# Kernel optimization log

Hardware: AMD Instinct MI355X
Metric: run time of the kernel (lower is better)

Reference implementation:

```python
import jax, jax.numpy as jnp
import numpy as np

T, DIM, HID = 8192, 1024, 4096

def setup_inputs() -> dict:
    key = jax.random.key(0)
    k1, k2, k3 = jax.random.split(key, 3)
    x = jax.random.normal(k1, (T, DIM), dtype=jnp.float32)
    # torch Linear weight layout: [out_features, in_features]
    W_fc = jax.random.normal(k2, (HID, DIM), dtype=jnp.float32) * 0.02
    W_proj = jax.random.normal(k3, (DIM, HID), dtype=jnp.float32) * 0.02
    return {"x": x, "W_fc": W_fc, "W_proj": W_proj}

def reference(x, W_fc, W_proj):
    # fc: x @ W_fc^T  -> relu -> square -> proj: @ W_proj^T
    h = jnp.einsum('td,hd->th', x, W_fc)      # [T, HID]
    h = jnp.square(jax.nn.relu(h))            # relu(h)^2 (relu^2 activation)
    return jnp.einsum('th,dh->td', h, W_proj) # [T, DIM]
```

## Files before the change

kernel.cpp:

```cpp
#include <hip/hip_runtime.h>
#include <stdint.h>


typedef __attribute__((ext_vector_type(8))) short bf16x8;
typedef __attribute__((ext_vector_type(4))) float f32x4;

typedef const __attribute__((address_space(1))) unsigned int* gas_u32p;
typedef __attribute__((address_space(3))) unsigned int* las_u32p;

__device__ __forceinline__ void load16_to_lds(const void* gptr, void* lptr) {
    __builtin_amdgcn_global_load_lds((gas_u32p)gptr, (las_u32p)lptr, 16, 0, 0);
}

__device__ __forceinline__ void dsr128(bf16x8& d, unsigned off) {
    asm volatile("ds_read_b128 %0, %1" : "=v"(d) : "v"(off));
}

__device__ __forceinline__ unsigned short f2bf(float f) {
    unsigned int u = __float_as_uint(f);
    u += 0x7FFFu + ((u >> 16) & 1u);
    return (unsigned short)(u >> 16);
}

__global__ void cvt_all(const float4* __restrict__ x,  ushort4* __restrict__ xb,
                        const float4* __restrict__ wf, ushort4* __restrict__ wfb,
                        const float4* __restrict__ wp, ushort4* __restrict__ wpb)
{
    const int base = blockIdx.x * 1024 + threadIdx.x;
    #pragma unroll
    for (int j = 0; j < 4; j++) {
        const int i = base + j * 256;
        const float4* s; ushort4* d; int k;
        if (i < (1 << 21))            { s = x;  d = xb;  k = i; }
        else if (i < 3 * (1 << 20))   { s = wf; d = wfb; k = i - (1 << 21); }
        else                          { s = wp; d = wpb; k = i - 3 * (1 << 20); }
        float4 v = s[k];
        ushort4 o;
        o.x = f2bf(v.x); o.y = f2bf(v.y); o.z = f2bf(v.z); o.w = f2bf(v.w);
        d[k] = o;
    }
}

#define LGKM0_FENCE() do { \
    asm volatile("s_waitcnt lgkmcnt(0)" ::: "memory"); \
    __builtin_amdgcn_sched_barrier(0); } while (0)

template<int NF, bool RELU2, bool OUT_BF16>
__global__ __launch_bounds__(512, 2)
void gemm8p(const unsigned short* __restrict__ A,
            const unsigned short* __restrict__ B,
            void* __restrict__ Cv, int M, int N, int K)
{
    constexpr int BM   = 256;
    constexpr int BN   = 64 * NF;
    constexpr int CB   = BN / 128;
    constexpr int AKH  = 16384;
    constexpr int BKH  = BN * 64;
    constexpr int BOFF = 2 * AKH;
    constexpr int BUFB = 2 * AKH + 2 * BKH;
    constexpr int KEEP = 2 + 2 * CB;
    (void)M;

    __shared__ char lds[2 * BUFB];

    const int tid  = threadIdx.x;
    const int lane = tid & 63;
    const int wave = tid >> 6;
    const int wm   = wave >> 2;
    const int wn   = wave & 3;
    const int quad = lane >> 4;
    const int m16  = lane & 15;

    const int gx = gridDim.x;
    int flat = blockIdx.y * gx + blockIdx.x;
    const int cpx = (gx * gridDim.y) >> 3;
    flat = (flat & 7) * cpx + (flat >> 3);
    const long bm0 = (long)(flat / gx) * BM;
    const long bn0 = (long)(flat % gx) * BN;

    const int srow   = tid >> 2;
    const int schunk = (tid & 3) ^ ((tid >> 3) & 3);
    const unsigned short* gA = A + (bm0 + srow) * (long)K + schunk * 8;
    const unsigned short* gB = B + (bn0 + srow) * (long)K + schunk * 8;
    char* lbase = (char*)lds;

    int offA[8], offB[NF];
    #pragma unroll
    for (int i = 0; i < 8; i++) {
        const int lo = (wm * 128 + i * 16 + m16) * 64 + quad * 16;
        offA[i] = lo ^ (((lo >> 7) & 3) << 4);
    }
    #pragma unroll
    for (int j = 0; j < NF; j++) {
        const int lo = (wn * 16 * NF + j * 16 + m16) * 64 + quad * 16;
        offB[j] = lo ^ (((lo >> 7) & 3) << 4);
    }

    f32x4 acc[8][NF];
    #pragma unroll
    for (int i = 0; i < 8; i++)
        #pragma unroll
        for (int j = 0; j < NF; j++)
            acc[i][j] = (f32x4)0.0f;

    const int NT = K >> 6;

    #define STAGE_A(t, kh) do { \
        char* _d = lbase + ((t) & 1) * BUFB + (kh) * AKH + tid * 16; \
        const unsigned short* _s = gA + (long)(t) * 64 + (kh) * 32; \
        load16_to_lds(_s, _d); \
        load16_to_lds(_s + 128l * K, _d + 8192); } while (0)

    #define STAGE_B(t, kh) do { \
        char* _d = lbase + ((t) & 1) * BUFB + BOFF + (kh) * BKH + tid * 16; \
        const unsigned short* _s = gB + (long)(t) * 64 + (kh) * 32; \
        load16_to_lds(_s, _d); \
        if (CB == 2) load16_to_lds(_s + 128l * K, _d + 8192); } while (0)

    STAGE_B(0, 0); STAGE_A(0, 0); STAGE_B(0, 1); STAGE_A(0, 1);
    if (NT > 1) {
        STAGE_B(1, 0); STAGE_A(1, 0); STAGE_B(1, 1);
        asm volatile("s_waitcnt vmcnt(%0)" :: "i"(KEEP) : "memory");
    } else {
        asm volatile("s_waitcnt vmcnt(0)" ::: "memory");
    }
    __builtin_amdgcn_sched_barrier(0);
    __builtin_amdgcn_s_barrier();

    for (int t = 0; t < NT; ++t) {
        char* bufA = lbase + (t & 1) * BUFB;
        char* bufB = bufA + BOFF;
        bf16x8 af[4], bf[NF];

        #pragma unroll
        for (int j = 0; j < NF; j++) bf[j] = *(const bf16x8*)(bufB + offB[j]);
        #pragma unroll
        for (int i = 0; i < 4; i++)  af[i] = *(const bf16x8*)(bufA + offA[i]);
        if (t + 1 < NT) STAGE_A(t + 1, 1);
        __builtin_amdgcn_s_barrier();
        LGKM0_FENCE();
        __builtin_amdgcn_s_setprio(1);
        #pragma unroll
        for (int i = 0; i < 4; i++)
            #pragma unroll
            for (int j = 0; j < NF; j++)
                acc[i][j] = __builtin_amdgcn_mfma_f32_16x16x32_bf16(
                    af[i], bf[j], acc[i][j], 0, 0, 0);
        __builtin_amdgcn_s_setprio(0);
        __builtin_amdgcn_s_barrier();

        #pragma unroll
        for (int i = 0; i < 4; i++)  af[i] = *(const bf16x8*)(bufA + offA[4 + i]);
        if (t + 2 < NT) STAGE_B(t + 2, 0);
        __builtin_amdgcn_s_barrier();
        LGKM0_FENCE();
        __builtin_amdgcn_s_setprio(1);
        #pragma unroll
        for (int i = 0; i < 4; i++)
            #pragma unroll
            for (int j = 0; j < NF; j++)
                acc[4 + i][j] = __builtin_amdgcn_mfma_f32_16x16x32_bf16(
                    af[i], bf[j], acc[4 + i][j], 0, 0, 0);
        __builtin_amdgcn_s_setprio(0);
        __builtin_amdgcn_s_barrier();

        #pragma unroll
        for (int j = 0; j < NF; j++) bf[j] = *(const bf16x8*)(bufB + BKH + offB[j]);
        #pragma unroll
        for (int i = 0; i < 4; i++)  af[i] = *(const bf16x8*)(bufA + AKH + offA[i]);
        if (t + 2 < NT) STAGE_A(t + 2, 0);
        __builtin_amdgcn_s_barrier();
        LGKM0_FENCE();
        __builtin_amdgcn_s_setprio(1);
        #pragma unroll
        for (int i = 0; i < 4; i++)
            #pragma unroll
            for (int j = 0; j < NF; j++)
                acc[i][j] = __builtin_amdgcn_mfma_f32_16x16x32_bf16(
                    af[i], bf[j], acc[i][j], 0, 0, 0);
        __builtin_amdgcn_s_setprio(0);
        __builtin_amdgcn_s_barrier();

        #pragma unroll
        for (int i = 0; i < 4; i++)  af[i] = *(const bf16x8*)(bufA + AKH + offA[4 + i]);
        if (t + 2 < NT) STAGE_B(t + 2, 1);
        __builtin_amdgcn_s_barrier();
        LGKM0_FENCE();
        __builtin_amdgcn_s_setprio(1);
        #pragma unroll
        for (int i = 0; i < 4; i++)
            #pragma unroll
            for (int j = 0; j < NF; j++)
                acc[4 + i][j] = __builtin_amdgcn_mfma_f32_16x16x32_bf16(
                    af[i], bf[j], acc[4 + i][j], 0, 0, 0);
        __builtin_amdgcn_s_setprio(0);
        if (t + 2 < NT) asm volatile("s_waitcnt vmcnt(%0)" :: "i"(KEEP) : "memory");
        else            asm volatile("s_waitcnt vmcnt(0)" ::: "memory");
        __builtin_amdgcn_sched_barrier(0);
        __builtin_amdgcn_s_barrier();
    }
    #undef STAGE_A
    #undef STAGE_B

    const long baseRow = bm0 + wm * 128 + quad * 4;
    const long baseCol = bn0 + wn * 16 * NF + m16;
    #pragma unroll
    for (int i = 0; i < 8; i++) {
        #pragma unroll
        for (int j = 0; j < NF; j++) {
            #pragma unroll
            for (int r = 0; r < 4; r++) {
                float v = acc[i][j][r];
                if (RELU2) v = (v > 0.0f) ? v * v : 0.0f;
                const long row = baseRow + i * 16 + r;
                const long col = baseCol + j * 16;
                if (OUT_BF16)
                    ((unsigned short*)Cv)[row * (long)N + col] = f2bf(v);
                else
                    ((float*)Cv)[row * (long)N + col] = v;
            }
        }
    }
}

__global__ __launch_bounds__(512, 2)
void gemm_skew(const unsigned short* __restrict__ A,
               const unsigned short* __restrict__ B,
               float* __restrict__ C, int M, int N, int K)
{
    constexpr int AKH  = 16384;
    constexpr int BKH  = 8192;
    constexpr int BOFF = 2 * AKH;
    constexpr int BUFB = 2 * AKH + 2 * BKH;
    (void)M;

    __shared__ char lds[2 * BUFB];

    const int tid  = threadIdx.x;
    const int lane = tid & 63;
    const int wave = tid >> 6;
    const int wm   = wave >> 1;
    const int wn   = wave & 1;
    const int quad = lane >> 4;
    const int m16  = lane & 15;

    const int gx = gridDim.x;
    int flat = blockIdx.y * gx + blockIdx.x;
    const int cpx = (gx * gridDim.y) >> 3;
    flat = (flat & 7) * cpx + (flat >> 3);
    const long bm0 = (long)(flat / gx) * 256;
    const long bn0 = (long)(flat % gx) * 128;

    const int srow   = tid >> 2;
    const int schunk = (tid & 3) ^ ((tid >> 3) & 3);
    const unsigned short* gA = A + (bm0 + srow) * (long)K + schunk * 8;
    const unsigned short* gB = B + (bn0 + srow) * (long)K + schunk * 8;

    unsigned offA[4], offB[4];
    #pragma unroll
    for (int i = 0; i < 4; i++) {
        const unsigned lo = (unsigned)((wm * 64 + i * 16 + m16) * 64 + quad * 16);
        offA[i] = lo ^ (((lo >> 7) & 3) << 4);
    }
    #pragma unroll
    for (int j = 0; j < 4; j++) {
        const unsigned lo = (unsigned)((wn * 64 + j * 16 + m16) * 64 + quad * 16);
        offB[j] = lo ^ (((lo >> 7) & 3) << 4);
    }

    const unsigned ldsbase =
        (unsigned)(unsigned long long)(las_u32p)(void*)lds;

    f32x4 acc[4][4];
    #pragma unroll
    for (int i = 0; i < 4; i++)
        #pragma unroll
        for (int j = 0; j < 4; j++)
            acc[i][j] = (f32x4)0.0f;

    const int NT = K >> 6;

    #define STAGE2(t, kh) do { \
        char* _dA = (char*)lds + ((t) & 1) * BUFB + (kh) * AKH + tid * 16; \
        const unsigned short* _sA = gA + (long)(t) * 64 + (kh) * 32; \
        load16_to_lds(_sA, _dA); \
        load16_to_lds(_sA + 128l * K, _dA + 8192); \
        char* _dB = (char*)lds + ((t) & 1) * BUFB + BOFF + (kh) * BKH + tid * 16; \
        load16_to_lds(gB + (long)(t) * 64 + (kh) * 32, _dB); } while (0)

    STAGE2(0, 0); STAGE2(0, 1);
    if (NT > 1) {
        STAGE2(1, 0);
        asm volatile("s_waitcnt vmcnt(3)" ::: "memory");
    } else {
        asm volatile("s_waitcnt vmcnt(0)" ::: "memory");
    }
    __builtin_amdgcn_sched_barrier(0);
    __builtin_amdgcn_s_barrier();

    for (int t = 0; t < NT; ++t) {
        const unsigned bufo = ldsbase + (unsigned)((t & 1) * BUFB);
        bf16x8 a0[4], b0[4], a1[4], b1[4];

        #pragma unroll
        for (int i = 0; i < 4; i++) dsr128(a0[i], bufo + offA[i]);
        #pragma unroll
        for (int j = 0; j < 4; j++) dsr128(b0[j], bufo + BOFF + offB[j]);
        #pragma unroll
        for (int i = 0; i < 4; i++) dsr128(a1[i], bufo + AKH + offA[i]);
        #pragma unroll
        for (int j = 0; j < 4; j++) dsr128(b1[j], bufo + BOFF + BKH + offB[j]);
        if (t + 1 < NT) STAGE2(t + 1, 1);
        __builtin_amdgcn_s_barrier();
        asm volatile("s_waitcnt lgkmcnt(8)" ::: "memory");
        __builtin_amdgcn_sched_barrier(0);
        __builtin_amdgcn_s_setprio(1);
        #pragma unroll
        for (int i = 0; i < 4; i++)
            #pragma unroll
            for (int j = 0; j < 4; j++)
                acc[i][j] = __builtin_amdgcn_mfma_f32_16x16x32_bf16(
                    a0[i], b0[j], acc[i][j], 0, 0, 0);
        __builtin_amdgcn_s_setprio(0);
        __builtin_amdgcn_s_barrier();

        if (t + 2 < NT) STAGE2(t + 2, 0);
        asm volatile("s_waitcnt lgkmcnt(0)" ::: "memory");
        __builtin_amdgcn_sched_barrier(0);
        __builtin_amdgcn_s_setprio(1);
        #pragma unroll
        for (int i = 0; i < 4; i++)
            #pragma unroll
            for (int j = 0; j < 4; j++)
                acc[i][j] = __builtin_amdgcn_mfma_f32_16x16x32_bf16(
                    a1[i], b1[j], acc[i][j], 0, 0, 0);
        __builtin_amdgcn_s_setprio(0);
        if (t + 2 < NT) asm volatile("s_waitcnt vmcnt(3)" ::: "memory");
        else            asm volatile("s_waitcnt vmcnt(0)" ::: "memory");
        __builtin_amdgcn_sched_barrier(0);
        __builtin_amdgcn_s_barrier();
    }
    #undef STAGE2

    const long baseRow = bm0 + wm * 64 + quad * 4;
    const long baseCol = bn0 + wn * 64 + m16;
    #pragma unroll
    for (int i = 0; i < 4; i++) {
        #pragma unroll
        for (int j = 0; j < 4; j++) {
            #pragma unroll
            for (int r = 0; r < 4; r++) {
                const long row = baseRow + i * 16 + r;
                const long col = baseCol + j * 16;
                C[row * (long)N + col] = acc[i][j][r];
            }
        }
    }
}

extern "C" void kernel_launch(void* const* d_in, const int* in_sizes, int n_in,
                              void* d_out, int out_size, void* d_ws, size_t ws_size,
                              hipStream_t stream) {
    (void)in_sizes; (void)n_in; (void)out_size; (void)ws_size;

    const int T = 8192, DIM = 1024, HID = 4096;

    const float* x     = (const float*)d_in[0];
    const float* W_fc  = (const float*)d_in[1];
    const float* W_prj = (const float*)d_in[2];
    float* out = (float*)d_out;

    char* ws = (char*)d_ws;
    unsigned short* h   = (unsigned short*)ws;
    unsigned short* xb  = (unsigned short*)(ws + (64l << 20));
    unsigned short* wfb = (unsigned short*)(ws + (80l << 20));
    unsigned short* wpb = (unsigned short*)(ws + (88l << 20));

    cvt_all<<<4096, 256, 0, stream>>>(
        (const float4*)x,     (ushort4*)xb,
        (const float4*)W_fc,  (ushort4*)wfb,
        (const float4*)W_prj, (ushort4*)wpb);

    gemm8p<4, true, true><<<dim3(HID / 256, T / 256), dim3(512), 0, stream>>>(
        xb, wfb, h, T, HID, DIM);

    gemm_skew<<<dim3(DIM / 128, T / 256), dim3(512), 0, stream>>>(
        h, wpb, out, T, DIM, HID);
}
```

Before: 242.6 us.

## Replace first GEMM with skewed pipeline using partial LDS waits

The templated first GEMM is replaced by a dedicated 256x256 kernel. It issues all LDS fragment reads up front with inline ds_read_b128 and waits with partial lgkmcnt counts, so MFMAs start before every read completes. It also merges the A and B staging into one macro and cuts the number of workgroup barriers per K-step from eight to three. In exchange it holds more fragment registers live at once, which raises register pressure and relies on hand-counted wait values being correct.

```diff
diff --git a/kernel.cpp b/kernel.cpp
--- a/kernel.cpp
+++ b/kernel.cpp
@@ -21,6 +21,13 @@
     u += 0x7FFFu + ((u >> 16) & 1u);
     return (unsigned short)(u >> 16);
 }
+
+#define LGKM(n) do { \
+    asm volatile("s_waitcnt lgkmcnt(%0)" :: "i"(n) : "memory"); \
+    __builtin_amdgcn_sched_barrier(0); } while (0)
+#define VMC(n) do { \
+    asm volatile("s_waitcnt vmcnt(%0)" :: "i"(n) : "memory"); \
+    __builtin_amdgcn_sched_barrier(0); } while (0)
 
 __global__ void cvt_all(const float4* __restrict__ x,  ushort4* __restrict__ xb,
                         const float4* __restrict__ wf, ushort4* __restrict__ wfb,
@@ -41,24 +48,15 @@
     }
 }
 
-#define LGKM0_FENCE() do { \
-    asm volatile("s_waitcnt lgkmcnt(0)" ::: "memory"); \
-    __builtin_amdgcn_sched_barrier(0); } while (0)
-
-template<int NF, bool RELU2, bool OUT_BF16>
 __global__ __launch_bounds__(512, 2)
-void gemm8p(const unsigned short* __restrict__ A,
-            const unsigned short* __restrict__ B,
-            void* __restrict__ Cv, int M, int N, int K)
+void gemm_skew1(const unsigned short* __restrict__ A,
+                const unsigned short* __restrict__ B,
+                unsigned short* __restrict__ C, int M, int N, int K)
 {
-    constexpr int BM   = 256;
-    constexpr int BN   = 64 * NF;
-    constexpr int CB   = BN / 128;
     constexpr int AKH  = 16384;
-    constexpr int BKH  = BN * 64;
+    constexpr int BKH  = 16384;
     constexpr int BOFF = 2 * AKH;
     constexpr int BUFB = 2 * AKH + 2 * BKH;
-    constexpr int KEEP = 2 + 2 * CB;
     (void)M;
 
     __shared__ char lds[2 * BUFB];
@@ -75,149 +73,139 @@
     int flat = blockIdx.y * gx + blockIdx.x;
     const int cpx = (gx * gridDim.y) >> 3;
     flat = (flat & 7) * cpx + (flat >> 3);
-    const long bm0 = (long)(flat / gx) * BM;
-    const long bn0 = (long)(flat % gx) * BN;
+    const long bm0 = (long)(flat / gx) * 256;
+    const long bn0 = (long)(flat % gx) * 256;
 
     const int srow   = tid >> 2;
     const int schunk = (tid & 3) ^ ((tid >> 3) & 3);
     const unsigned short* gA = A + (bm0 + srow) * (long)K + schunk * 8;
     const unsigned short* gB = B + (bn0 + srow) * (long)K + schunk * 8;
-    char* lbase = (char*)lds;
-
-    int offA[8], offB[NF];
+
+    unsigned offA[8], offB[4];
     #pragma unroll
     for (int i = 0; i < 8; i++) {
-        const int lo = (wm * 128 + i * 16 + m16) * 64 + quad * 16;
+        const unsigned lo = (unsigned)((wm * 128 + i * 16 + m16) * 64 + quad * 16);
         offA[i] = lo ^ (((lo >> 7) & 3) << 4);
     }
     #pragma unroll
-    for (int j = 0; j < NF; j++) {
-        const int lo = (wn * 16 * NF + j * 16 + m16) * 64 + quad * 16;
+    for (int j = 0; j < 4; j++) {
+        const unsigned lo = (unsigned)((wn * 64 + j * 16 + m16) * 64 + quad * 16);
         offB[j] = lo ^ (((lo >> 7) & 3) << 4);
     }
 
-    f32x4 acc[8][NF];
+    const unsigned ldsbase =
+        (unsigned)(unsigned long long)(las_u32p)(void*)lds;
+
+    f32x4 acc[8][4];
     #pragma unroll
     for (int i = 0; i < 8; i++)
         #pragma unroll
-        for (int j = 0; j < NF; j++)
+        for (int j = 0; j < 4; j++)
             acc[i][j] = (f32x4)0.0f;
 
     const int NT = K >> 6;
 
-    #define STAGE_A(t, kh) do { \
-        char* _d = lbase + ((t) & 1) * BUFB + (kh) * AKH + tid * 16; \
-        const unsigned short* _s = gA + (long)(t) * 64 + (kh) * 32; \
-        load16_to_lds(_s, _d); \
-        load16_to_lds(_s + 128l * K, _d + 8192); } while (0)
-
-    #define STAGE_B(t, kh) do { \
-        char* _d = lbase + ((t) & 1) * BUFB + BOFF + (kh) * BKH + tid * 16; \
-        const unsigned short* _s = gB + (long)(t) * 64 + (kh) * 32; \
-        load16_to_lds(_s, _d); \
-        if (CB == 2) load16_to_lds(_s + 128l * K, _d + 8192); } while (0)
-
-    STAGE_B(0, 0); STAGE_A(0, 0); STAGE_B(0, 1); STAGE_A(0, 1);
+    #define STG1(t, kh) do { \
+        char* _dA = (char*)lds + ((t) & 1) * BUFB + (kh) * AKH + tid * 16; \
+        const unsigned short* _sA = gA + (long)(t) * 64 + (kh) * 32; \
+        load16_to_lds(_sA, _dA); \
+        load16_to_lds(_sA + 128l * K, _dA + 8192); \
+        char* _dB = (char*)lds + ((t) & 1) * BUFB + BOFF + (kh) * BKH + tid * 16; \
+        const unsigned short* _sB = gB + (long)(t) * 64 + (kh) * 32; \
+        load16_to_lds(_sB, _dB); \
+        load16_to_lds(_sB + 128l * K, _dB + 8192); } while (0)
+
+    STG1(0, 0); STG1(0, 1);
     if (NT > 1) {
-        STAGE_B(1, 0); STAGE_A(1, 0); STAGE_B(1, 1);
-        asm volatile("s_waitcnt vmcnt(%0)" :: "i"(KEEP) : "memory");
+        STG1(1, 0);
+        VMC(4);
     } else {
-        asm volatile("s_waitcnt vmcnt(0)" ::: "memory");
-    }
-    __builtin_amdgcn_sched_barrier(0);
+        VMC(0);
+    }
     __builtin_amdgcn_s_barrier();
 
     for (int t = 0; t < NT; ++t) {
-        char* bufA = lbase + (t & 1) * BUFB;
-        char* bufB = bufA + BOFF;
-        bf16x8 af[4], bf[NF];
-
-        #pragma unroll
-        for (int j = 0; j < NF; j++) bf[j] = *(const bf16x8*)(bufB + offB[j]);
-        #pragma unroll
-        for (int i = 0; i < 4; i++)  af[i] = *(const bf16x8*)(bufA + offA[i]);
-        if (t + 1 < NT) STAGE_A(t + 1, 1);
-        __builtin_amdgcn_s_barrier();
-        LGKM0_FENCE();
-        __builtin_amdgcn_s_setprio(1);
-        #pragma unroll
-        for (int i = 0; i < 4; i++)
-            #pragma unroll
-            for (int j = 0; j < NF; j++)
+        const unsigned bufo = ldsbase + (unsigned)((t & 1) * BUFB);
+        bf16x8 a0[4], b0[4], a0b[4], a1[4], b1[4], a1b[4];
+
+        #pragma unroll
+        for (int i = 0; i < 4; i++) dsr128(a0[i],  bufo + offA[i]);
+        #pragma unroll
+        for (int j = 0; j < 4; j++) dsr128(b0[j],  bufo + BOFF + offB[j]);
+        #pragma unroll
+        for (int i = 0; i < 4; i++) dsr128(a0b[i], bufo + offA[4 + i]);
+        if (t + 1 < NT) STG1(t + 1, 1);
+        __builtin_amdgcn_s_barrier();
+
+        LGKM(4);
+        __builtin_amdgcn_s_setprio(1);
+        #pragma unroll
+        for (int i = 0; i < 4; i++)
+            #pragma unroll
+            for (int j = 0; j < 4; j++)
                 acc[i][j] = __builtin_amdgcn_mfma_f32_16x16x32_bf16(
-                    af[i], bf[j], acc[i][j], 0, 0, 0);
-        __builtin_amdgcn_s_setprio(0);
-        __builtin_amdgcn_s_barrier();
-
-        #pragma unroll
-        for (int i = 0; i < 4; i++)  af[i] = *(const bf16x8*)(bufA + offA[4 + i]);
-        if (t + 2 < NT) STAGE_B(t + 2, 0);
-        __builtin_amdgcn_s_barrier();
-        LGKM0_FENCE();
-        __builtin_amdgcn_s_setprio(1);
-        #pragma unroll
-        for (int i = 0; i < 4; i++)
-            #pragma unroll
-            for (int j = 0; j < NF; j++)
+                    a0[i], b0[j], acc[i][j], 0, 0, 0);
+        __builtin_amdgcn_s_setprio(0);
+
+        #pragma unroll
+        for (int i = 0; i < 4; i++) dsr128(a1[i],  bufo + AKH + offA[i]);
+        #pragma unroll
+        for (int j = 0; j < 4; j++) dsr128(b1[j],  bufo + BOFF + BKH + offB[j]);
+        #pragma unroll
+        for (int i = 0; i < 4; i++) dsr128(a1b[i], bufo + AKH + offA[4 + i]);
+
+        LGKM(12);
+        __builtin_amdgcn_s_setprio(1);
+        #pragma unroll
+        for (int i = 0; i < 4; i++)
+            #pragma unroll
+            for (int j = 0; j < 4; j++)
                 acc[4 + i][j] = __builtin_amdgcn_mfma_f32_16x16x32_bf16(
-                    af[i], bf[j], acc[4 + i][j], 0, 0, 0);
-        __builtin_amdgcn_s_setprio(0);
-        __builtin_amdgcn_s_barrier();
-
-        #pragma unroll
-        for (int j = 0; j < NF; j++) bf[j] = *(const bf16x8*)(bufB + BKH + offB[j]);
-        #pragma unroll
-        for (int i = 0; i < 4; i++)  af[i] = *(const bf16x8*)(bufA + AKH + offA[i]);
-        if (t + 2 < NT) STAGE_A(t + 2, 0);
-        __builtin_amdgcn_s_barrier();
-        LGKM0_FENCE();
-        __builtin_amdgcn_s_setprio(1);
-        #pragma unroll
-        for (int i = 0; i < 4; i++)
-            #pragma unroll
-            for (int j = 0; j < NF; j++)
+                    a0b[i], b0[j], acc[4 + i][j], 0, 0, 0);
+        __builtin_amdgcn_s_setprio(0);
+        __builtin_amdgcn_s_barrier();
+
+        if (t + 2 < NT) STG1(t + 2, 0);
+
+        LGKM(4);
+        __builtin_amdgcn_s_setprio(1);
+        #pragma unroll
+        for (int i = 0; i < 4; i++)
+            #pragma unroll
+            for (int j = 0; j < 4; j++)
                 acc[i][j] = __builtin_amdgcn_mfma_f32_16x16x32_bf16(
-                    af[i], bf[j], acc[i][j], 0, 0, 0);
-        __builtin_amdgcn_s_setprio(0);
-        __builtin_amdgcn_s_barrier();
-
-        #pragma unroll
-        for (int i = 0; i < 4; i++)  af[i] = *(const bf16x8*)(bufA + AKH + offA[4 + i]);
-        if (t + 2 < NT) STAGE_B(t + 2, 1);
-        __builtin_amdgcn_s_barrier();
-        LGKM0_FENCE();
-        __builtin_amdgcn_s_setprio(1);
-        #pragma unroll
-        for (int i = 0; i < 4; i++)
-            #pragma unroll
-            for (int j = 0; j < NF; j++)
+                    a1[i], b1[j], acc[i][j], 0, 0, 0);
+        __builtin_amdgcn_s_setprio(0);
+
+        LGKM(0);
+        __builtin_amdgcn_s_setprio(1);
+        #pragma unroll
+        for (int i = 0; i < 4; i++)
+            #pragma unroll
+            for (int j = 0; j < 4; j++)
                 acc[4 + i][j] = __builtin_amdgcn_mfma_f32_16x16x32_bf16(
-                    af[i], bf[j], acc[4 + i][j], 0, 0, 0);
-        __builtin_amdgcn_s_setprio(0);
-        if (t + 2 < NT) asm volatile("s_waitcnt vmcnt(%0)" :: "i"(KEEP) : "memory");
-        else            asm volatile("s_waitcnt vmcnt(0)" ::: "memory");
-        __builtin_amdgcn_sched_barrier(0);
-        __builtin_amdgcn_s_barrier();
-    }
-    #undef STAGE_A
-    #undef STAGE_B
+                    a1b[i], b1[j], acc[4 + i][j], 0, 0, 0);
+        __builtin_amdgcn_s_setprio(0);
+
+        if (t + 2 < NT) VMC(4);
+        else            VMC(0);
+        __builtin_amdgcn_s_barrier();
+    }
+    #undef STG1
 
     const long baseRow = bm0 + wm * 128 + quad * 4;
-    const long baseCol = bn0 + wn * 16 * NF + m16;
+    const long baseCol = bn0 + wn * 64 + m16;
     #pragma unroll
     for (int i = 0; i < 8; i++) {
         #pragma unroll
-        for (int j = 0; j < NF; j++) {
+        for (int j = 0; j < 4; j++) {
             #pragma unroll
             for (int r = 0; r < 4; r++) {
                 float v = acc[i][j][r];
-                if (RELU2) v = (v > 0.0f) ? v * v : 0.0f;
+                v = (v > 0.0f) ? v * v : 0.0f;
                 const long row = baseRow + i * 16 + r;
                 const long col = baseCol + j * 16;
-                if (OUT_BF16)
-                    ((unsigned short*)Cv)[row * (long)N + col] = f2bf(v);
-                else
-                    ((float*)Cv)[row * (long)N + col] = v;
+                C[row * (long)N + col] = f2bf(v);
             }
         }
     }
@@ -381,7 +369,7 @@
         (const float4*)W_fc,  (ushort4*)wfb,
         (const float4*)W_prj, (ushort4*)wpb);
 
-    gemm8p<4, true, true><<<dim3(HID / 256, T / 256), dim3(512), 0, stream>>>(
+    gemm_skew1<<<dim3(HID / 256, T / 256), dim3(512), 0, stream>>>(
         xb, wfb, h, T, HID, DIM);
 
     gemm_skew<<<dim3(DIM / 128, T / 256), dim3(512), 0, stream>>>(
```

Measured after the change: 241.0 us. About the same (-0.7%).
